# Optimization experiments

Hardware: AMD Instinct MI355X
Metric: run time of the kernel (lower is better)

The kernel has to match this reference:

```python
import math
import jax, jax.numpy as jnp
import numpy as np

B, C, T = 8, 512, 4096
DK = max(C // 8, 2)          # 64
SCALE = math.sqrt(DK)        # 8.0
GAMMA = 1.0                  # source inits gamma=0 (identity); use 1.0 to exercise the attention path
EPS = 1e-12


def _l2_normalize(v):
    return v / (jnp.linalg.norm(v) + EPS)


def setup_inputs() -> dict:
    key = jax.random.key(0)
    ks = jax.random.split(key, 5)
    return {
        "x": jax.random.normal(ks[0], (B, C, T), jnp.float32),
        "Wq": jax.random.normal(ks[1], (DK, C), jnp.float32) * 0.05,
        "Wk": jax.random.normal(ks[2], (DK, C), jnp.float32) * 0.05,
        "Wv": jax.random.normal(ks[3], (C, C), jnp.float32) * 0.05,
        "bv": jnp.zeros((C,), jnp.float32),
        "u": jax.random.normal(ks[4], (C,), jnp.float32),
    }


def reference(x, Wq, Wk, Wv, bv, u):
    # spectral norm on value conv weight (one power iteration, u/v as buffers)
    v = jax.lax.stop_gradient(_l2_normalize(Wv.T @ u))
    u2 = jax.lax.stop_gradient(_l2_normalize(Wv @ v))
    sigma = u2 @ (Wv @ v)
    Wv_sn = Wv / sigma

    # 1x1 conv projections
    q = jnp.einsum('dc,bct->btd', Wq, x)               # [B,T,DK]
    k = jnp.einsum('dc,bct->bdt', Wk, x)               # [B,DK,T]
    energy = jnp.einsum('btd,bds->bts', q, k) / SCALE  # [B,T,T]
    attn = jax.nn.softmax(energy, axis=-1)
    val = jnp.einsum('oc,bct->bot', Wv_sn, x) + bv[None, :, None]  # [B,C,T]
    # out = bmm(value, attention^T): out[b,c,t] = sum_s val[b,c,s]*attn[b,t,s]
    out = jnp.einsum('bcs,bts->bct', val, attn)        # [B,C,T]
    return GAMMA * out + x
```

## Files before the change

kernel.cpp:

```cpp
#include <hip/hip_runtime.h>


#define B_  8
#define C_  512
#define T_  4096
#define DK_ 64

typedef __bf16 bf16x8 __attribute__((ext_vector_type(8)));
typedef float  f32x4  __attribute__((ext_vector_type(4)));

static __device__ __forceinline__ unsigned short f2bf(float f) {
  unsigned u = __float_as_uint(f);
  u += 0x7fffu + ((u >> 16) & 1u);
  return (unsigned short)(u >> 16);
}

__global__ void sigma_kernel(const float* __restrict__ Wv,
                             const float* __restrict__ u,
                             float* __restrict__ sig) {
  __shared__ float red[512];
  __shared__ float vsh[512];
  __shared__ float snorm;
  int tid = threadIdx.x;

  vsh[tid] = u[tid];
  __syncthreads();
  float acc = 0.f;
  for (int j = 0; j < 512; ++j) acc += Wv[(size_t)j * 512 + tid] * vsh[j];
  red[tid] = acc * acc;
  __syncthreads();
  for (int s = 256; s >= 1; s >>= 1) {
    if (tid < s) red[tid] += red[tid + s];
    __syncthreads();
  }
  if (tid == 0) snorm = sqrtf(red[0]) + 1e-12f;
  __syncthreads();
  float v = acc / snorm;
  __syncthreads();
  vsh[tid] = v;
  __syncthreads();
  float wacc = 0.f;
  for (int c = 0; c < 512; ++c) wacc += Wv[(size_t)tid * 512 + c] * vsh[c];
  red[tid] = wacc * wacc;
  __syncthreads();
  for (int s = 256; s >= 1; s >>= 1) {
    if (tid < s) red[tid] += red[tid + s];
    __syncthreads();
  }
  if (tid == 0) {
    float ww = red[0];
    float sigma = ww / (sqrtf(ww) + 1e-12f);
    sig[0] = 1.f / sigma;
  }
}

__global__ __launch_bounds__(128)
void castw_kernel(const float* __restrict__ Wq, const float* __restrict__ Wk,
                  const float* __restrict__ Wv, const float* __restrict__ sig,
                  unsigned short* __restrict__ Wc) {
  int row = blockIdx.x;
  int c = threadIdx.x * 4;
  const float* src;
  float s;
  if (row < 64) {
    src = Wq + (size_t)row * 512;
    s = 1.4426950408889634f / 8.0f;
  } else if (row < 128) {
    src = Wk + (size_t)(row - 64) * 512;
    s = 1.0f;
  } else {
    src = Wv + (size_t)(row - 128) * 512;
    s = sig[0];
  }
  float4 v = *reinterpret_cast<const float4*>(src + c);
  ushort4 o;
  o.x = f2bf(v.x * s);
  o.y = f2bf(v.y * s);
  o.z = f2bf(v.z * s);
  o.w = f2bf(v.w * s);
  *reinterpret_cast<ushort4*>(Wc + (size_t)row * 512 + c) = o;
}

__global__ __launch_bounds__(256)
void castt_kernel(const float* __restrict__ x, unsigned short* __restrict__ xT) {
  __shared__ __align__(16) unsigned short ldsT[64][72];
  int tid = threadIdx.x;
  int t0 = blockIdx.x * 64, c0 = blockIdx.y * 64, b = blockIdx.z;
  const float* xb = x + ((size_t)b * C_ + c0) * T_ + t0;
#pragma unroll
  for (int k2 = 0; k2 < 4; ++k2) {
    int idx = k2 * 256 + tid;
    int c = idx >> 4, t4 = (idx & 15) * 4;
    float4 v = *reinterpret_cast<const float4*>(xb + (size_t)c * T_ + t4);
    ldsT[t4 + 0][c] = f2bf(v.x);
    ldsT[t4 + 1][c] = f2bf(v.y);
    ldsT[t4 + 2][c] = f2bf(v.z);
    ldsT[t4 + 3][c] = f2bf(v.w);
  }
  __syncthreads();
  unsigned short* xTb = xT + ((size_t)b * T_ + t0) * C_ + c0;
#pragma unroll
  for (int k2 = 0; k2 < 2; ++k2) {
    int idx = k2 * 256 + tid;
    int t = idx >> 3, ch = idx & 7;
    bf16x8 v = *reinterpret_cast<const bf16x8*>(&ldsT[t][ch * 8]);
    *reinterpret_cast<bf16x8*>(xTb + (size_t)t * C_ + ch * 8) = v;
  }
}

__global__ __launch_bounds__(512, 2)
void proj_kernel(const unsigned short* __restrict__ Wc,
                 const unsigned short* __restrict__ xT,
                 const float* __restrict__ bv,
                 unsigned short* __restrict__ Q,
                 unsigned short* __restrict__ Kk,
                 unsigned short* __restrict__ V) {
  __shared__ __align__(16) char smem[98304];
  const int tid = threadIdx.x;
  const int w = tid >> 6;
  const int lane = tid & 63;
  const int col = lane & 15;
  const int g = lane >> 4;
  const int b = blockIdx.x & 7;
  const int t0 = (blockIdx.x >> 3) * 128;

  const unsigned short* xTb = xT + ((size_t)b * T_ + t0) * C_;

  auto stageX = [&](int bsel, int kc) {
    int off = w * 1024 + lane * 16;
    int tl = off >> 6;
    int cb = off & 63;
    const unsigned short* src = xTb + (size_t)tl * C_ + kc + cb / 2;
    __builtin_amdgcn_global_load_lds(
        (const __attribute__((address_space(1))) unsigned int*)src,
        (__attribute__((address_space(3))) unsigned int*)(smem + bsel * 8192 + off),
        16, 0, 0);
  };
  auto stageW = [&](int bsel, int kc) {
#pragma unroll
    for (int i = 0; i < 5; ++i) {
      int off = i * 8192 + w * 1024 + lane * 16;
      int o = off >> 6;
      int cb = off & 63;
      const unsigned short* src = Wc + (size_t)o * 512 + kc + cb / 2;
      __builtin_amdgcn_global_load_lds(
          (const __attribute__((address_space(1))) unsigned int*)src,
          (__attribute__((address_space(3))) unsigned int*)(smem + 16384 + bsel * 40960 + off),
          16, 0, 0);
    }
  };

  f32x4 acc[5][8];
#pragma unroll
  for (int of = 0; of < 5; ++of)
#pragma unroll
    for (int j = 0; j < 8; ++j) acc[of][j] = (f32x4){0.f, 0.f, 0.f, 0.f};

  stageX(0, 0);
  stageW(0, 0);
  __syncthreads();
  int cur = 0;

  for (int ks = 0; ks < 16; ++ks) {
    int kc = ks * 32;
    if (ks < 15) {
      stageX(cur ^ 1, kc + 32);
      stageW(cur ^ 1, kc + 32);
    }
    bf16x8 af[5], bfr[8];
#pragma unroll
    for (int of = 0; of < 5; ++of) {
      int o = w * 80 + of * 16 + col;
      af[of] = *reinterpret_cast<const bf16x8*>(smem + 16384 + cur * 40960 + o * 64 + g * 16);
    }
#pragma unroll
    for (int j = 0; j < 8; ++j) {
      int tl = 16 * j + col;
      bfr[j] = *reinterpret_cast<const bf16x8*>(smem + cur * 8192 + tl * 64 + g * 16);
    }
#pragma unroll
    for (int of = 0; of < 5; ++of)
#pragma unroll
      for (int j = 0; j < 8; ++j)
        acc[of][j] = __builtin_amdgcn_mfma_f32_16x16x32_bf16(af[of], bfr[j], acc[of][j], 0, 0, 0);
    __syncthreads();
    cur ^= 1;
  }

  unsigned short* qkt = (unsigned short*)smem;
  unsigned short* vt = (unsigned short*)(smem + 34816 + w * 4352);
  unsigned short* Vb = V + (size_t)b * C_ * T_;

#pragma unroll
  for (int of = 0; of < 5; ++of) {
    int o0 = w * 80 + of * 16;
    if (o0 < 128) {
#pragma unroll
      for (int j = 0; j < 8; ++j)
#pragma unroll
        for (int r = 0; r < 4; ++r)
          qkt[(16 * j + col) * 136 + o0 + g * 4 + r] = f2bf(acc[of][j][r]);
    } else {
      int c0 = o0 - 128;
      float bvr[4];
#pragma unroll
      for (int r = 0; r < 4; ++r) bvr[r] = bv[c0 + g * 4 + r];
#pragma unroll
      for (int j = 0; j < 8; ++j)
#pragma unroll
        for (int r = 0; r < 4; ++r)
          vt[(g * 4 + r) * 136 + 16 * j + col] = f2bf(acc[of][j][r] + bvr[r]);
#pragma unroll
      for (int p = 0; p < 4; ++p) {
        int o_r = p * 4 + g;
        bf16x8 v8 = *reinterpret_cast<const bf16x8*>((char*)vt + o_r * 272 + col * 16);
        *reinterpret_cast<bf16x8*>(Vb + (size_t)(c0 + o_r) * T_ + t0 + col * 8) = v8;
      }
    }
  }
  __syncthreads();
  unsigned short* Qb = Q + (size_t)b * T_ * DK_;
  unsigned short* Kb = Kk + (size_t)b * T_ * DK_;
#pragma unroll
  for (int k2 = 0; k2 < 2; ++k2) {
    int idx = k2 * 512 + tid;
    int t = idx >> 3, ch = idx & 7;
    bf16x8 q8 = *reinterpret_cast<const bf16x8*>(&qkt[t * 136 + ch * 8]);
    *reinterpret_cast<bf16x8*>(Qb + (size_t)(t0 + t) * DK_ + ch * 8) = q8;
    bf16x8 k8 = *reinterpret_cast<const bf16x8*>(&qkt[t * 136 + 64 + ch * 8]);
    *reinterpret_cast<bf16x8*>(Kb + (size_t)(t0 + t) * DK_ + ch * 8) = k8;
  }
}

__global__ __launch_bounds__(512, 2)
void flash_kernel(const unsigned short* __restrict__ Q,
                  const unsigned short* __restrict__ Kk,
                  const unsigned short* __restrict__ V,
                  const float* __restrict__ x, float* __restrict__ out) {
  __shared__ __align__(16) unsigned short v_lds[2][C_ * 64];
  __shared__ __align__(16) unsigned short p_lds[8][16 * 64];

  const int tid = threadIdx.x;
  const int w = tid >> 6;
  const int lane = tid & 63;
  const int col = lane & 15;
  const int g = lane >> 4;
  const int bid = blockIdx.x;
  const int b = bid & 7;
  const int t0 = (bid >> 3) * 128;
  const int trow0 = t0 + w * 16;

  const unsigned short* Qb = Q + (size_t)b * T_ * DK_;
  const unsigned short* Kb = Kk + (size_t)b * T_ * DK_;
  const unsigned short* Vb = V + (size_t)b * C_ * T_;

  auto stage = [&](int bsel, int s0) {
#pragma unroll
    for (int i = 0; i < 8; ++i) {
      int o = i * 8192 + tid * 16;
      int c = o >> 7;
      int z = (o & 127) ^ ((c & 7) << 4);
      const unsigned short* src = Vb + (size_t)c * T_ + s0 + (z >> 1);
      void* dst = (char*)(&v_lds[bsel][0]) + i * 8192 + w * 1024;
      __builtin_amdgcn_global_load_lds(
          (const __attribute__((address_space(1))) unsigned int*)src,
          (__attribute__((address_space(3))) unsigned int*)dst, 16, 0, 0);
    }
  };

  bf16x8 qf[2];
  {
    const unsigned short* qrow = Qb + (size_t)(trow0 + col) * DK_ + g * 8;
    qf[0] = *reinterpret_cast<const bf16x8*>(qrow);
    qf[1] = *reinterpret_cast<const bf16x8*>(qrow + 32);
  }

  bf16x8 kf[2][4];
  auto loadK = [&](int s0) {
#pragma unroll
    for (int ks = 0; ks < 2; ++ks)
#pragma unroll
      for (int j = 0; j < 4; ++j)
        kf[ks][j] = *reinterpret_cast<const bf16x8*>(
            Kb + (size_t)(s0 + col + 16 * j) * DK_ + 32 * ks + g * 8);
  };

  float m_r[4], l_r[4];
  f32x4 o_acc[32];
#pragma unroll
  for (int n = 0; n < 32; ++n) o_acc[n] = (f32x4){0.f, 0.f, 0.f, 0.f};
#pragma unroll
  for (int r = 0; r < 4; ++r) { m_r[r] = -1e30f; l_r[r] = 0.f; }

  stage(0, 0);
  loadK(0);
  __syncthreads();
  int cur = 0;

  const float RTHR = 10.0f;

  for (int it = 0; it < T_ / 64; ++it) {
    const int s0 = it * 64;
    if (it + 1 < T_ / 64) stage(cur ^ 1, s0 + 64);

    f32x4 sacc[4];
#pragma unroll
    for (int j = 0; j < 4; ++j) sacc[j] = (f32x4){0.f, 0.f, 0.f, 0.f};
#pragma unroll
    for (int ks = 0; ks < 2; ++ks)
#pragma unroll
      for (int j = 0; j < 4; ++j)
        sacc[j] = __builtin_amdgcn_mfma_f32_16x16x32_bf16(qf[ks], kf[ks][j], sacc[j], 0, 0, 0);

    float mx[4];
#pragma unroll
    for (int r = 0; r < 4; ++r) {
      float m2 = fmaxf(fmaxf(sacc[0][r], sacc[1][r]), fmaxf(sacc[2][r], sacc[3][r]));
      m2 = fmaxf(m2, __shfl_xor(m2, 1));
      m2 = fmaxf(m2, __shfl_xor(m2, 2));
      m2 = fmaxf(m2, __shfl_xor(m2, 4));
      m2 = fmaxf(m2, __shfl_xor(m2, 8));
      mx[r] = m2;
    }
    int ok = (mx[0] <= m_r[0] + RTHR) && (mx[1] <= m_r[1] + RTHR) &&
             (mx[2] <= m_r[2] + RTHR) && (mx[3] <= m_r[3] + RTHR);
    if (!__all(ok)) {
      float scl[4];
#pragma unroll
      for (int r = 0; r < 4; ++r) {
        float mnew = fmaxf(m_r[r], mx[r]);
        scl[r] = exp2f(m_r[r] - mnew);
        m_r[r] = mnew;
        l_r[r] *= scl[r];
      }
#pragma unroll
      for (int n = 0; n < 32; ++n) {
        o_acc[n][0] *= scl[0];
        o_acc[n][1] *= scl[1];
        o_acc[n][2] *= scl[2];
        o_acc[n][3] *= scl[3];
      }
    }
#pragma unroll
    for (int r = 0; r < 4; ++r) {
      float rs = 0.f;
#pragma unroll
      for (int j = 0; j < 4; ++j) {
        float p = exp2f(sacc[j][r] - m_r[r]);
        sacc[j][r] = p;
        rs += p;
      }
      rs += __shfl_xor(rs, 1);
      rs += __shfl_xor(rs, 2);
      rs += __shfl_xor(rs, 4);
      rs += __shfl_xor(rs, 8);
      l_r[r] += rs;
    }

#pragma unroll
    for (int j = 0; j < 4; ++j)
#pragma unroll
      for (int r = 0; r < 4; ++r) {
        int row = g * 4 + r;
        int byteoff = (row * 128 + (16 * j + col) * 2) ^ ((row & 7) << 4);
        *(unsigned short*)((char*)p_lds[w] + byteoff) = f2bf(sacc[j][r]);
      }

#pragma unroll
    for (int ks = 0; ks < 2; ++ks) {
      int bo = (col * 128 + 64 * ks + 16 * g) ^ ((col & 7) << 4);
      bf16x8 pf = *reinterpret_cast<const bf16x8*>((char*)p_lds[w] + bo);
      int zv = (64 * ks + 16 * g) ^ ((col & 7) << 4);
      const char* vb0 = (const char*)v_lds[cur] + col * 128 + zv;
#pragma unroll
      for (int n = 0; n < 32; ++n) {
        bf16x8 vf = *reinterpret_cast<const bf16x8*>(vb0 + n * 2048);
        o_acc[n] = __builtin_amdgcn_mfma_f32_16x16x32_bf16(pf, vf, o_acc[n], 0, 0, 0);
      }
    }

    if (it + 1 < T_ / 64) loadK(s0 + 64);
    __syncthreads();
    cur ^= 1;
  }

  float inv_l[4];
#pragma unroll
  for (int r = 0; r < 4; ++r) inv_l[r] = 1.f / l_r[r];
  const float* xb = x + (size_t)b * C_ * T_;
  float* ob = out + (size_t)b * C_ * T_;
  float* scratch = (float*)((char*)v_lds + (size_t)w * 16384);

#pragma unroll
  for (int ch = 0; ch < 4; ++ch) {
#pragma unroll
    for (int nn = 0; nn < 8; ++nn) {
      int n = ch * 8 + nn;
      int c_local = nn * 16 + col;
#pragma unroll
      for (int r = 0; r < 4; ++r)
        scratch[c_local * 17 + g * 4 + r] = o_acc[n][r] * inv_l[r];
    }
#pragma unroll
    for (int i = 0; i < 32; ++i) {
      int c_local = i * 4 + g;
      float v = scratch[c_local * 17 + col];
      size_t idx = (size_t)(ch * 128 + c_local) * T_ + trow0 + col;
      ob[idx] = v + xb[idx];
    }
  }
}

extern "C" void kernel_launch(void* const* d_in, const int* in_sizes, int n_in,
                              void* d_out, int out_size, void* d_ws, size_t ws_size,
                              hipStream_t stream) {
  const float* x  = (const float*)d_in[0];
  const float* Wq = (const float*)d_in[1];
  const float* Wk = (const float*)d_in[2];
  const float* Wv = (const float*)d_in[3];
  const float* bv = (const float*)d_in[4];
  const float* u  = (const float*)d_in[5];
  float* out = (float*)d_out;

  char* ws = (char*)d_ws;
  float* sig = (float*)ws;
  unsigned short* Q  = (unsigned short*)(ws + 1024);
  unsigned short* Kk = (unsigned short*)(ws + 1024 + (size_t)4 * 1024 * 1024);
  unsigned short* V  = (unsigned short*)(ws + 1024 + (size_t)8 * 1024 * 1024);
  unsigned short* xT = (unsigned short*)(ws + 1024 + (size_t)40 * 1024 * 1024);
  unsigned short* Wc = (unsigned short*)(ws + 1024 + (size_t)72 * 1024 * 1024);

  sigma_kernel<<<1, 512, 0, stream>>>(Wv, u, sig);
  castw_kernel<<<640, 128, 0, stream>>>(Wq, Wk, Wv, sig, Wc);
  castt_kernel<<<dim3(T_ / 64, C_ / 64, B_), 256, 0, stream>>>(x, xT);
  proj_kernel<<<256, 512, 0, stream>>>(Wc, xT, bv, Q, Kk, V);
  flash_kernel<<<256, 512, 0, stream>>>(Q, Kk, V, x, out);
}
```

Measured before the change: 369.4 us.

## Repartition PV matmul so each wave owns channel slice across all query rows

The PV stage is restructured. Previously each wave held all 512 output channels for its own 16 query rows. Now each wave owns 64 channels for all 128 query rows, and P is shared through a block-wide LDS buffer. This cuts the redundant V fragment reads from LDS, since each wave reads only its channel slice, and lets the epilogue store f32x4 vectors directly without a scratch transpose. The cost is a cross-wave handshake: per-wave rescale flags and scales go through LDS, and each iteration now needs two barriers, with a manual vmcnt wait replacing the single __syncthreads.

```diff
diff --git a/kernel.cpp b/kernel.cpp
--- a/kernel.cpp
+++ b/kernel.cpp
@@ -14,6 +14,8 @@
   u += 0x7fffu + ((u >> 16) & 1u);
   return (unsigned short)(u >> 16);
 }
+
+#define BAR_LDS() asm volatile("s_waitcnt lgkmcnt(0)\ns_barrier" ::: "memory")
 
 __global__ void sigma_kernel(const float* __restrict__ Wv,
                              const float* __restrict__ u,
@@ -238,16 +240,18 @@
                   const unsigned short* __restrict__ V,
                   const float* __restrict__ x, float* __restrict__ out) {
   __shared__ __align__(16) unsigned short v_lds[2][C_ * 64];
-  __shared__ __align__(16) unsigned short p_lds[8][16 * 64];
+  __shared__ __align__(16) unsigned short p_lds[128 * 64];
+  __shared__ __align__(16) float scale_lds[8][16];
+  __shared__ __align__(16) float l_lds[128];
+  __shared__ unsigned long long flags_lds;
 
   const int tid = threadIdx.x;
   const int w = tid >> 6;
   const int lane = tid & 63;
   const int col = lane & 15;
   const int g = lane >> 4;
-  const int bid = blockIdx.x;
-  const int b = bid & 7;
-  const int t0 = (bid >> 3) * 128;
+  const int b = blockIdx.x & 7;
+  const int t0 = (blockIdx.x >> 3) * 128;
   const int trow0 = t0 + w * 16;
 
   const unsigned short* Qb = Q + (size_t)b * T_ * DK_;
@@ -274,7 +278,6 @@
     qf[0] = *reinterpret_cast<const bf16x8*>(qrow);
     qf[1] = *reinterpret_cast<const bf16x8*>(qrow + 32);
   }
-
   bf16x8 kf[2][4];
   auto loadK = [&](int s0) {
 #pragma unroll
@@ -285,12 +288,12 @@
             Kb + (size_t)(s0 + col + 16 * j) * DK_ + 32 * ks + g * 8);
   };
 
-  float m_r[4], l_r[4];
-  f32x4 o_acc[32];
-#pragma unroll
-  for (int n = 0; n < 32; ++n) o_acc[n] = (f32x4){0.f, 0.f, 0.f, 0.f};
-#pragma unroll
-  for (int r = 0; r < 4; ++r) { m_r[r] = -1e30f; l_r[r] = 0.f; }
+  float m_run = -1e30f, l_run = 0.f;
+  f32x4 o_acc[8][4];
+#pragma unroll
+  for (int qt = 0; qt < 8; ++qt)
+#pragma unroll
+    for (int ct = 0; ct < 4; ++ct) o_acc[qt][ct] = (f32x4){0.f, 0.f, 0.f, 0.f};
 
   stage(0, 0);
   loadK(0);
@@ -298,11 +301,10 @@
   int cur = 0;
 
   const float RTHR = 10.0f;
+  const int prow = w * 16 + col;
+  const int pswz = (prow & 7) << 4;
 
   for (int it = 0; it < T_ / 64; ++it) {
-    const int s0 = it * 64;
-    if (it + 1 < T_ / 64) stage(cur ^ 1, s0 + 64);
-
     f32x4 sacc[4];
 #pragma unroll
     for (int j = 0; j < 4; ++j) sacc[j] = (f32x4){0.f, 0.f, 0.f, 0.f};
@@ -310,103 +312,106 @@
     for (int ks = 0; ks < 2; ++ks)
 #pragma unroll
       for (int j = 0; j < 4; ++j)
-        sacc[j] = __builtin_amdgcn_mfma_f32_16x16x32_bf16(qf[ks], kf[ks][j], sacc[j], 0, 0, 0);
-
-    float mx[4];
-#pragma unroll
-    for (int r = 0; r < 4; ++r) {
-      float m2 = fmaxf(fmaxf(sacc[0][r], sacc[1][r]), fmaxf(sacc[2][r], sacc[3][r]));
-      m2 = fmaxf(m2, __shfl_xor(m2, 1));
-      m2 = fmaxf(m2, __shfl_xor(m2, 2));
-      m2 = fmaxf(m2, __shfl_xor(m2, 4));
-      m2 = fmaxf(m2, __shfl_xor(m2, 8));
-      mx[r] = m2;
-    }
-    int ok = (mx[0] <= m_r[0] + RTHR) && (mx[1] <= m_r[1] + RTHR) &&
-             (mx[2] <= m_r[2] + RTHR) && (mx[3] <= m_r[3] + RTHR);
-    if (!__all(ok)) {
-      float scl[4];
-#pragma unroll
-      for (int r = 0; r < 4; ++r) {
-        float mnew = fmaxf(m_r[r], mx[r]);
-        scl[r] = exp2f(m_r[r] - mnew);
-        m_r[r] = mnew;
-        l_r[r] *= scl[r];
+        sacc[j] = __builtin_amdgcn_mfma_f32_16x16x32_bf16(kf[ks][j], qf[ks], sacc[j], 0, 0, 0);
+
+    float t01 = fmaxf(fmaxf(sacc[0][0], sacc[0][1]), fmaxf(sacc[0][2], sacc[0][3]));
+    float t23 = fmaxf(fmaxf(sacc[1][0], sacc[1][1]), fmaxf(sacc[1][2], sacc[1][3]));
+    float t45 = fmaxf(fmaxf(sacc[2][0], sacc[2][1]), fmaxf(sacc[2][2], sacc[2][3]));
+    float t67 = fmaxf(fmaxf(sacc[3][0], sacc[3][1]), fmaxf(sacc[3][2], sacc[3][3]));
+    float tm = fmaxf(fmaxf(t01, t23), fmaxf(t45, t67));
+    tm = fmaxf(tm, __shfl_xor(tm, 16));
+    tm = fmaxf(tm, __shfl_xor(tm, 32));
+    int wave_any = __any(tm > m_run + RTHR);
+    float sc = 1.0f;
+    if (wave_any) {
+      float m_new = fmaxf(m_run, tm);
+      sc = exp2f(m_run - m_new);
+      m_run = m_new;
+      if (lane < 16) scale_lds[w][lane] = sc;
+    }
+    if (lane == 0)
+      ((volatile unsigned char*)&flags_lds)[w] = (unsigned char)wave_any;
+
+    BAR_LDS();
+
+    unsigned long long fl = flags_lds;
+    if (fl) {
+#pragma unroll
+      for (int qt = 0; qt < 8; ++qt) {
+        if ((fl >> (8 * qt)) & 0xffull) {
+          f32x4 s4 = *reinterpret_cast<const f32x4*>(&scale_lds[qt][4 * g]);
+#pragma unroll
+          for (int ct = 0; ct < 4; ++ct) o_acc[qt][ct] *= s4;
+        }
       }
-#pragma unroll
-      for (int n = 0; n < 32; ++n) {
-        o_acc[n][0] *= scl[0];
-        o_acc[n][1] *= scl[1];
-        o_acc[n][2] *= scl[2];
-        o_acc[n][3] *= scl[3];
+    }
+
+    float rs = 0.f;
+#pragma unroll
+    for (int j = 0; j < 4; ++j) {
+      float p0 = exp2f(sacc[j][0] - m_run);
+      float p1 = exp2f(sacc[j][1] - m_run);
+      float p2 = exp2f(sacc[j][2] - m_run);
+      float p3 = exp2f(sacc[j][3] - m_run);
+      rs += (p0 + p1) + (p2 + p3);
+      ushort4 pk = {f2bf(p0), f2bf(p1), f2bf(p2), f2bf(p3)};
+      int byteoff = prow * 128 + (((16 * j + 4 * g) * 2) ^ pswz);
+      *reinterpret_cast<ushort4*>((char*)p_lds + byteoff) = pk;
+    }
+    rs += __shfl_xor(rs, 16);
+    rs += __shfl_xor(rs, 32);
+    l_run = l_run * sc + rs;
+
+    if (it + 1 < T_ / 64) {
+      loadK(64 * (it + 1));
+      stage(cur ^ 1, 64 * (it + 1));
+    }
+
+    BAR_LDS();
+    asm volatile("s_waitcnt vmcnt(16)" ::: "memory");
+
+    const char* vbase = (const char*)v_lds[cur];
+#pragma unroll
+    for (int ks = 0; ks < 2; ++ks) {
+      bf16x8 vf[4];
+#pragma unroll
+      for (int ct = 0; ct < 4; ++ct) {
+        int c_ = 64 * w + 16 * ct + col;
+        vf[ct] = *reinterpret_cast<const bf16x8*>(
+            vbase + c_ * 128 + ((64 * ks + 16 * g) ^ ((c_ & 7) << 4)));
       }
-    }
-#pragma unroll
-    for (int r = 0; r < 4; ++r) {
-      float rs = 0.f;
-#pragma unroll
-      for (int j = 0; j < 4; ++j) {
-        float p = exp2f(sacc[j][r] - m_r[r]);
-        sacc[j][r] = p;
-        rs += p;
+#pragma unroll
+      for (int qt = 0; qt < 8; ++qt) {
+        int row = 16 * qt + col;
+        bf16x8 pa = *reinterpret_cast<const bf16x8*>(
+            (const char*)p_lds + row * 128 + ((64 * ks + 16 * g) ^ ((row & 7) << 4)));
+#pragma unroll
+        for (int ct = 0; ct < 4; ++ct)
+          o_acc[qt][ct] = __builtin_amdgcn_mfma_f32_16x16x32_bf16(pa, vf[ct], o_acc[qt][ct], 0, 0, 0);
       }
-      rs += __shfl_xor(rs, 1);
-      rs += __shfl_xor(rs, 2);
-      rs += __shfl_xor(rs, 4);
-      rs += __shfl_xor(rs, 8);
-      l_r[r] += rs;
-    }
-
-#pragma unroll
-    for (int j = 0; j < 4; ++j)
-#pragma unroll
-      for (int r = 0; r < 4; ++r) {
-        int row = g * 4 + r;
-        int byteoff = (row * 128 + (16 * j + col) * 2) ^ ((row & 7) << 4);
-        *(unsigned short*)((char*)p_lds[w] + byteoff) = f2bf(sacc[j][r]);
-      }
-
-#pragma unroll
-    for (int ks = 0; ks < 2; ++ks) {
-      int bo = (col * 128 + 64 * ks + 16 * g) ^ ((col & 7) << 4);
-      bf16x8 pf = *reinterpret_cast<const bf16x8*>((char*)p_lds[w] + bo);
-      int zv = (64 * ks + 16 * g) ^ ((col & 7) << 4);
-      const char* vb0 = (const char*)v_lds[cur] + col * 128 + zv;
-#pragma unroll
-      for (int n = 0; n < 32; ++n) {
-        bf16x8 vf = *reinterpret_cast<const bf16x8*>(vb0 + n * 2048);
-        o_acc[n] = __builtin_amdgcn_mfma_f32_16x16x32_bf16(pf, vf, o_acc[n], 0, 0, 0);
-      }
-    }
-
-    if (it + 1 < T_ / 64) loadK(s0 + 64);
-    __syncthreads();
+    }
     cur ^= 1;
   }
 
-  float inv_l[4];
-#pragma unroll
-  for (int r = 0; r < 4; ++r) inv_l[r] = 1.f / l_r[r];
+  if (lane < 16) l_lds[w * 16 + lane] = l_run;
+  BAR_LDS();
+
   const float* xb = x + (size_t)b * C_ * T_;
   float* ob = out + (size_t)b * C_ * T_;
-  float* scratch = (float*)((char*)v_lds + (size_t)w * 16384);
-
-#pragma unroll
-  for (int ch = 0; ch < 4; ++ch) {
-#pragma unroll
-    for (int nn = 0; nn < 8; ++nn) {
-      int n = ch * 8 + nn;
-      int c_local = nn * 16 + col;
-#pragma unroll
-      for (int r = 0; r < 4; ++r)
-        scratch[c_local * 17 + g * 4 + r] = o_acc[n][r] * inv_l[r];
-    }
-#pragma unroll
-    for (int i = 0; i < 32; ++i) {
-      int c_local = i * 4 + g;
-      float v = scratch[c_local * 17 + col];
-      size_t idx = (size_t)(ch * 128 + c_local) * T_ + trow0 + col;
-      ob[idx] = v + xb[idx];
+#pragma unroll
+  for (int qt = 0; qt < 8; ++qt) {
+    f32x4 l4 = *reinterpret_cast<const f32x4*>(&l_lds[16 * qt + 4 * g]);
+    f32x4 linv;
+#pragma unroll
+    for (int r = 0; r < 4; ++r) linv[r] = 1.f / l4[r];
+#pragma unroll
+    for (int ct = 0; ct < 4; ++ct) {
+      size_t idx = (size_t)(64 * w + 16 * ct + col) * T_ + t0 + 16 * qt + 4 * g;
+      f32x4 xv = *reinterpret_cast<const f32x4*>(xb + idx);
+      f32x4 o = o_acc[qt][ct];
+#pragma unroll
+      for (int r = 0; r < 4; ++r) o[r] = o[r] * linv[r] + xv[r];
+      *reinterpret_cast<f32x4*>(ob + idx) = o;
     }
   }
 }
```

Result: no change. 364.6 us (-1.3%).
